# Performance work log

Hardware: AMD Instinct MI355X
Metric: run time of the kernel (lower is better)

The kernel has to match this reference:

```python
import jax, jax.numpy as jnp
import numpy as np

B, NSEQ, SEQ_PER = 2, 4, 256
S = NSEQ * SEQ_PER            # total sequence (stocks interleaved along seq dim)
D, H, HD = 1024, 16, 64       # d_model, nhead, head_dim
HD2, HD4 = HD // 2, HD // 4
DFF = 4096
LAMBDA_INIT = 0.2             # lambda_init_fn(0) = 0.8 - 0.6*exp(0)
SCALING = 1.0 / float(np.sqrt(HD2))
EPS_DEF = float(np.finfo(np.float32).eps)   # torch RMSNorm default eps (eps=None)
EPS_ATTN = 1e-5


def _rms(x, w, eps):
    return x * jax.lax.rsqrt(jnp.mean(x * x, axis=-1, keepdims=True) + eps) * w


def _rope(x, fc):
    # x: (B, T, NSEQ, 2H, HD2); fc: (T, HD4, 2) holding (cos, sin)
    xr = x.reshape(x.shape[:-1] + (HD4, 2))
    c = fc[None, :, None, None, :, 0]
    s = fc[None, :, None, None, :, 1]
    x0, x1 = xr[..., 0], xr[..., 1]
    return jnp.stack([x0 * c - x1 * s, x0 * s + x1 * c], axis=-1).reshape(x.shape)


def setup_inputs():
    key = jax.random.key(0)
    ks = jax.random.split(key, 16)
    def w(i, shape, std=0.02):
        return jax.random.normal(ks[i], shape, jnp.float32) * std
    # true RoPE table for seq_per_stock-1 positions
    t = jnp.arange(SEQ_PER - 1, dtype=jnp.float32)[:, None]
    inv = 1.0 / (10000.0 ** (jnp.arange(HD4, dtype=jnp.float32) / HD4))
    ang = t * inv[None, :]
    return {
        "x": jax.random.normal(ks[0], (B, S, D), jnp.float32),
        "freqs_cis": jnp.stack([jnp.cos(ang), jnp.sin(ang)], axis=-1),
        "w_norm1": jnp.ones((D,), jnp.float32),
        "w_norm2": jnp.ones((D,), jnp.float32),
        "Wq": w(1, (H * HD, D)), "bq": jnp.zeros((H * HD,), jnp.float32),
        "Wk": w(2, (H * HD, D)), "bk": jnp.zeros((H * HD,), jnp.float32),
        "Wv": w(3, (H * HD, D)), "bv": jnp.zeros((H * HD,), jnp.float32),
        "Wo": w(4, (D, H * HD)), "bo": jnp.zeros((D,), jnp.float32),
        "lq1": w(5, (HD2,), 0.1), "lk1": w(6, (HD2,), 0.1),
        "lq2": w(7, (HD2,), 0.1), "lk2": w(8, (HD2,), 0.1),
        "w_attn_norm": jnp.ones((HD,), jnp.float32),
        "Wg": w(9, (2 * DFF, D)), "bg": jnp.zeros((2 * DFF,), jnp.float32),
        "Wout": w(10, (D, DFF)), "bout": jnp.zeros((D,), jnp.float32),
    }


def reference(x, freqs_cis, w_norm1, w_norm2, Wq, bq, Wk, bk, Wv, bv, Wo, bo,
              lq1, lk1, lq2, lk2, w_attn_norm, Wg, bg, Wout, bout):
    Bz, Sz, _ = x.shape
    h = _rms(x, w_norm1, EPS_DEF)
    q = (h @ Wq.T + bq).reshape(Bz, SEQ_PER, NSEQ, 2 * H, HD2)
    k = (h @ Wk.T + bk).reshape(Bz, SEQ_PER, NSEQ, 2 * H, HD2)
    v = (h @ Wv.T + bv).reshape(Bz, Sz, H, HD).transpose(0, 2, 1, 3)   # (B,H,S,HD), interleaved order
    # RoPE on all but the first per-stock timestep; same freqs for every stock
    q = jnp.concatenate([q[:, :1], _rope(q[:, 1:], freqs_cis)], axis=1)
    k = jnp.concatenate([k[:, :1], _rope(k[:, 1:], freqs_cis)], axis=1)
    # reorder q/k to stock-major flat sequence (torch permute(0,4,1,2,3)+reshape)
    q = q.transpose(0, 2, 1, 3, 4).reshape(Bz, Sz, 2 * H, HD2).transpose(0, 2, 1, 3)
    k = k.transpose(0, 2, 1, 3, 4).reshape(Bz, Sz, 2 * H, HD2).transpose(0, 2, 1, 3)
    scores = jnp.einsum('bhqd,bhkd->bhqk', q, k) * SCALING              # (B,2H,S,S)
    causal = jnp.triu(jnp.ones((SEQ_PER, SEQ_PER), bool), 1)
    mask = jnp.tile(causal, (NSEQ, NSEQ))   # block-tiled causal, as torch .repeat
    att = jnp.sign(scores) * jax.nn.softmax(
        jnp.where(mask, -1e30, jnp.abs(scores)), axis=-1)
    lam = jnp.exp(jnp.sum(lk1 * lq1)) - jnp.exp(jnp.sum(lk2 * lq2)) + LAMBDA_INIT
    att = att.reshape(Bz, H, 2, Sz, Sz)
    a1, a2 = att[:, :, 0], att[:, :, 1]
    G = jnp.mean(a1, axis=-2, keepdims=True)          # mean over queries, broadcast back
    a = jnp.where(mask, 0.0, a1 - lam * a2 + lam * G)
    ao = jnp.einsum('bhqk,bhkd->bhqd', a, v)          # v kept in interleaved order (faithful to source)
    ao = _rms(ao, w_attn_norm, EPS_ATTN)
    ao = ao.reshape(Bz, Sz, H * HD)  # flat reinterpret (B,H,S,HD)->(B,S,H*HD), matches torch reshape chain
    x = x + ao @ Wo.T + bo
    h2 = _rms(x, w_norm2, EPS_DEF)
    u, vg = jnp.split(h2 @ Wg.T + bg, 2, axis=-1)
    return x + (u * jax.nn.silu(vg)) @ Wout.T + bout
```

## Files before the change

### kernel.cpp

```cpp
#include <hip/hip_runtime.h>

#define LAMBDA_INIT 0.2f
#define SCALING 0.17677669529663687f
#define EPS_DEF 1.1920928955078125e-07f
#define EPS_ATTN 1e-5f

typedef unsigned short us4 __attribute__((ext_vector_type(4)));
typedef unsigned short us8v __attribute__((ext_vector_type(8)));
typedef float f32x4 __attribute__((ext_vector_type(4)));
typedef float f32x2 __attribute__((ext_vector_type(2)));
typedef __bf16 bf16x8 __attribute__((ext_vector_type(8)));

#define MFMA16(a, b, c) __builtin_amdgcn_mfma_f32_16x16x32_bf16((a), (b), (c), 0, 0, 0)

__device__ __forceinline__ float bf2f(unsigned short u) {
    unsigned int x = ((unsigned int)u) << 16;
    return __builtin_bit_cast(float, x);
}
__device__ __forceinline__ unsigned short f2bf(float f) {
    unsigned int x = __builtin_bit_cast(unsigned int, f);
    x += 0x7fffu + ((x >> 16) & 1u);
    return (unsigned short)(x >> 16);
}
__device__ __forceinline__ void split8(f32x4 a, f32x4 b, us8v& hi, us8v& lo) {
#pragma unroll
    for (int u = 0; u < 4; u++) {
        unsigned short h = f2bf(a[u]);
        hi[u] = h; lo[u] = f2bf(a[u] - bf2f(h));
        unsigned short h2 = f2bf(b[u]);
        hi[4 + u] = h2; lo[4 + u] = f2bf(b[u] - bf2f(h2));
    }
}
__device__ __forceinline__ bf16x8 ldb(const unsigned short* p) {
    return __builtin_bit_cast(bf16x8, *(const us8v*)p);
}

__device__ __forceinline__ float wave_sum(float v) {
#pragma unroll
    for (int o = 32; o > 0; o >>= 1) v += __shfl_down(v, o);
    return v;
}
__device__ __forceinline__ float block_sum(float v, float* red4) {
    int wv = threadIdx.x >> 6;
    float w = wave_sum(v);
    __syncthreads();
    if ((threadIdx.x & 63) == 0) red4[wv] = w;
    __syncthreads();
    return red4[0] + red4[1] + red4[2] + red4[3];
}

__global__ __launch_bounds__(256) void prep(float* __restrict__ G, float* __restrict__ lamp,
                                            const float* lq1, const float* lk1,
                                            const float* lq2, const float* lk2) {
    int i = (blockIdx.x * 256 + threadIdx.x) * 4;
    G[i] = 0.f; G[i + 1] = 0.f; G[i + 2] = 0.f; G[i + 3] = 0.f;
    if (blockIdx.x == 0 && threadIdx.x == 0) {
        float a = 0.f, c = 0.f;
        for (int d = 0; d < 32; d++) {
            a += lq1[d] * lk1[d];
            c += lq2[d] * lk2[d];
        }
        *lamp = expf(a) - expf(c) + LAMBDA_INIT;
    }
}

__global__ __launch_bounds__(256) void cvt_bf16(const float* __restrict__ s,
                                                unsigned short* __restrict__ d, int n4) {
    int i = blockIdx.x * 256 + threadIdx.x;
    if (i >= n4) return;
    f32x4 v = ((const f32x4*)s)[i];
    us4 o;
#pragma unroll
    for (int u = 0; u < 4; u++) o[u] = f2bf(v[u]);
    ((us4*)d)[i] = o;
}

__global__ __launch_bounds__(256) void cvt_split3(
        const float* __restrict__ s0, const float* __restrict__ s1, const float* __restrict__ s2,
        unsigned short* __restrict__ h0, unsigned short* __restrict__ l0,
        unsigned short* __restrict__ h1p, unsigned short* __restrict__ l1p,
        unsigned short* __restrict__ h2p, unsigned short* __restrict__ l2p, int n4) {
    const int z = blockIdx.y;
    const float* s = (z == 0) ? s0 : (z == 1) ? s1 : s2;
    unsigned short* hi = (z == 0) ? h0 : (z == 1) ? h1p : h2p;
    unsigned short* lo = (z == 0) ? l0 : (z == 1) ? l1p : l2p;
    int i = blockIdx.x * 256 + threadIdx.x;
    if (i >= n4) return;
    f32x4 v = ((const f32x4*)s)[i];
    us4 h, l;
#pragma unroll
    for (int u = 0; u < 4; u++) {
        h[u] = f2bf(v[u]);
        l[u] = f2bf(v[u] - bf2f(h[u]));
    }
    ((us4*)hi)[i] = h;
    ((us4*)lo)[i] = l;
}

template <int OUTBF>
__global__ __launch_bounds__(256) void rms_kernel(const float* __restrict__ x,
                                                  const float* __restrict__ w,
                                                  void* __restrict__ out, float eps) {
    int row = blockIdx.x;
    int tid = threadIdx.x;
    size_t base = (size_t)row * 1024 + tid * 4;
    f32x4 v = *(const f32x4*)(x + base);
    float ss = v[0]*v[0] + v[1]*v[1] + v[2]*v[2] + v[3]*v[3];
    __shared__ float red4[4];
    float tot = block_sum(ss, red4);
    float r = rsqrtf(tot * (1.0f / 1024.f) + eps);
    f32x4 wv = *(const f32x4*)(w + tid * 4);
    if (OUTBF) {
        us4 o;
#pragma unroll
        for (int i = 0; i < 4; i++) o[i] = f2bf(v[i] * r * wv[i]);
        *(us4*)((unsigned short*)out + base) = o;
    } else {
        f32x4 o;
#pragma unroll
        for (int i = 0; i < 4; i++) o[i] = v[i] * r * wv[i];
        *(f32x4*)((float*)out + base) = o;
    }
}

__global__ __launch_bounds__(256) void rms_split(const float* __restrict__ x,
                                                 const float* __restrict__ w,
                                                 unsigned short* __restrict__ hh,
                                                 unsigned short* __restrict__ hl, float eps) {
    int row = blockIdx.x;
    int tid = threadIdx.x;
    size_t base = (size_t)row * 1024 + tid * 4;
    f32x4 v = *(const f32x4*)(x + base);
    float ss = v[0]*v[0] + v[1]*v[1] + v[2]*v[2] + v[3]*v[3];
    __shared__ float red4[4];
    float tot = block_sum(ss, red4);
    float r = rsqrtf(tot * (1.0f / 1024.f) + eps);
    f32x4 wv = *(const f32x4*)(w + tid * 4);
    us4 oh, ol;
#pragma unroll
    for (int i = 0; i < 4; i++) {
        float val = v[i] * r * wv[i];
        oh[i] = f2bf(val);
        ol[i] = f2bf(val - bf2f(oh[i]));
    }
    *(us4*)(hh + base) = oh;
    *(us4*)(hl + base) = ol;
}

__global__ __launch_bounds__(256) void gemm_qkv_ps(
        const unsigned short* __restrict__ AH, const unsigned short* __restrict__ AL,
        const unsigned short* __restrict__ WqH, const unsigned short* __restrict__ WqL,
        const unsigned short* __restrict__ WkH, const unsigned short* __restrict__ WkL,
        const unsigned short* __restrict__ WvH, const unsigned short* __restrict__ WvL,
        const float* __restrict__ bq, const float* __restrict__ bk, const float* __restrict__ bv,
        float* __restrict__ Yq, float* __restrict__ Yk, float* __restrict__ Yv) {
    const int z = blockIdx.z;
    const unsigned short* BH = (z == 0) ? WqH : (z == 1) ? WkH : WvH;
    const unsigned short* BL = (z == 0) ? WqL : (z == 1) ? WkL : WvL;
    const float* bias = (z == 0) ? bq : (z == 1) ? bk : bv;
    float* out        = (z == 0) ? Yq : (z == 1) ? Yk : Yv;
    const int K = 1024, N = 1024;
    __shared__ __align__(16) unsigned short Ah[64][72];
    __shared__ __align__(16) unsigned short Al[64][72];
    __shared__ __align__(16) unsigned short Bh[64][72];
    __shared__ __align__(16) unsigned short Bl[64][72];
    const int t = threadIdx.x;
    const int bm = blockIdx.x, bn = blockIdx.y;
    const int lane = t & 63, w = t >> 6;
    const int wr = w >> 1, wc = w & 1;
    const int l15 = lane & 15, lg = lane >> 4;
    const int sr = t >> 2, sc = (t & 3) * 16;

    const unsigned short* AgH = AH + (size_t)(bm * 64 + sr) * K + sc;
    const unsigned short* AgL = AL + (size_t)(bm * 64 + sr) * K + sc;
    const unsigned short* BgH = BH + (size_t)(bn * 64 + sr) * K + sc;
    const unsigned short* BgL = BL + (size_t)(bn * 64 + sr) * K + sc;

    f32x4 acc[2][2] = {};

    us8v ah0 = *(const us8v*)AgH, ah1 = *(const us8v*)(AgH + 8);
    us8v al0 = *(const us8v*)AgL, al1 = *(const us8v*)(AgL + 8);
    us8v bh0 = *(const us8v*)BgH, bh1 = *(const us8v*)(BgH + 8);
    us8v bl0 = *(const us8v*)BgL, bl1 = *(const us8v*)(BgL + 8);

    for (int k0 = 0; k0 < K; k0 += 64) {
        __syncthreads();
        *(us8v*)&Ah[sr][sc] = ah0; *(us8v*)&Ah[sr][sc + 8] = ah1;
        *(us8v*)&Al[sr][sc] = al0; *(us8v*)&Al[sr][sc + 8] = al1;
        *(us8v*)&Bh[sr][sc] = bh0; *(us8v*)&Bh[sr][sc + 8] = bh1;
        *(us8v*)&Bl[sr][sc] = bl0; *(us8v*)&Bl[sr][sc + 8] = bl1;
        __syncthreads();
        if (k0 + 64 < K) {
            const int kn = k0 + 64;
            ah0 = *(const us8v*)(AgH + kn); ah1 = *(const us8v*)(AgH + kn + 8);
            al0 = *(const us8v*)(AgL + kn); al1 = *(const us8v*)(AgL + kn + 8);
            bh0 = *(const us8v*)(BgH + kn); bh1 = *(const us8v*)(BgH + kn + 8);
            bl0 = *(const us8v*)(BgL + kn); bl1 = *(const us8v*)(BgL + kn + 8);
        }
#pragma unroll
        for (int kk = 0; kk < 2; kk++) {
            bf16x8 afh[2], afl[2], bfh[2], bfl[2];
#pragma unroll
            for (int mi = 0; mi < 2; mi++) {
                afh[mi] = ldb(&Ah[wr * 32 + mi * 16 + l15][kk * 32 + lg * 8]);
                afl[mi] = ldb(&Al[wr * 32 + mi * 16 + l15][kk * 32 + lg * 8]);
            }
#pragma unroll
            for (int ni = 0; ni < 2; ni++) {
                bfh[ni] = ldb(&Bh[wc * 32 + ni * 16 + l15][kk * 32 + lg * 8]);
                bfl[ni] = ldb(&Bl[wc * 32 + ni * 16 + l15][kk * 32 + lg * 8]);
            }
#pragma unroll
            for (int mi = 0; mi < 2; mi++)
#pragma unroll
                for (int ni = 0; ni < 2; ni++) {
                    acc[mi][ni] = MFMA16(afl[mi], bfh[ni], acc[mi][ni]);
                    acc[mi][ni] = MFMA16(afh[mi], bfl[ni], acc[mi][ni]);
                    acc[mi][ni] = MFMA16(afh[mi], bfh[ni], acc[mi][ni]);
                }
        }
    }

    const int rbase = bm * 64 + wr * 32 + (lg << 2);
    const int cbase = bn * 64 + wc * 32 + l15;
#pragma unroll
    for (int mi = 0; mi < 2; mi++) {
#pragma unroll
        for (int ni = 0; ni < 2; ni++) {
            int col = cbase + ni * 16;
            float bb = bias[col];
#pragma unroll
            for (int r = 0; r < 4; r++) {
                int row = rbase + mi * 16 + r;
                out[(size_t)row * N + col] = acc[mi][ni][r] + bb;
            }
        }
    }
}

__global__ __launch_bounds__(256) void gemm_mfma_wb(const unsigned short* __restrict__ A,
                                                    const unsigned short* __restrict__ Bt,
                                                    const float* __restrict__ bias,
                                                    const float* __restrict__ res,
                                                    float* __restrict__ out,
                                                    int M, int N, int K) {
    __shared__ __align__(16) unsigned short As[64][72];
    __shared__ __align__(16) unsigned short Bs[64][72];
    const int t = threadIdx.x;
    const int bm = blockIdx.x, bn = blockIdx.y;
    const int lane = t & 63, w = t >> 6;
    const int wr = w >> 1, wc = w & 1;
    const int l15 = lane & 15, lg = lane >> 4;
    const int sr = t >> 2, sc = (t & 3) * 16;

    const unsigned short* Ag = A + (size_t)(bm * 64 + sr) * K + sc;
    const unsigned short* Bg = Bt + (size_t)(bn * 64 + sr) * K + sc;

    f32x4 acc[2][2] = {};

    us8v a0 = *(const us8v*)Ag, a1 = *(const us8v*)(Ag + 8);
    us8v b0 = *(const us8v*)Bg, b1 = *(const us8v*)(Bg + 8);

    for (int k0 = 0; k0 < K; k0 += 64) {
        __syncthreads();
        *(us8v*)&As[sr][sc]     = a0;
        *(us8v*)&As[sr][sc + 8] = a1;
        *(us8v*)&Bs[sr][sc]     = b0;
        *(us8v*)&Bs[sr][sc + 8] = b1;
        __syncthreads();
        if (k0 + 64 < K) {
            const int kn = k0 + 64;
            a0 = *(const us8v*)(Ag + kn); a1 = *(const us8v*)(Ag + kn + 8);
            b0 = *(const us8v*)(Bg + kn); b1 = *(const us8v*)(Bg + kn + 8);
        }
#pragma unroll
        for (int kk = 0; kk < 2; kk++) {
            bf16x8 af[2], bf[2];
#pragma unroll
            for (int mi = 0; mi < 2; mi++)
                af[mi] = ldb(&As[wr * 32 + mi * 16 + l15][kk * 32 + lg * 8]);
#pragma unroll
            for (int ni = 0; ni < 2; ni++)
                bf[ni] = ldb(&Bs[wc * 32 + ni * 16 + l15][kk * 32 + lg * 8]);
#pragma unroll
            for (int mi = 0; mi < 2; mi++)
#pragma unroll
                for (int ni = 0; ni < 2; ni++)
                    acc[mi][ni] = MFMA16(af[mi], bf[ni], acc[mi][ni]);
        }
    }

    const int rbase = bm * 64 + wr * 32 + (lg << 2);
    const int cbase = bn * 64 + wc * 32 + l15;
#pragma unroll
    for (int mi = 0; mi < 2; mi++) {
#pragma unroll
        for (int ni = 0; ni < 2; ni++) {
            int col = cbase + ni * 16;
            float bb = bias[col];
#pragma unroll
            for (int r = 0; r < 4; r++) {
                int row = rbase + mi * 16 + r;
                size_t oi = (size_t)row * N + col;
                out[oi] = acc[mi][ni][r] + bb + res[oi];
            }
        }
    }
}

__global__ __launch_bounds__(256) void gemm_gate_wb(const unsigned short* __restrict__ A,
                                                    const unsigned short* __restrict__ WuB,
                                                    const unsigned short* __restrict__ WvB,
                                                    const float* __restrict__ bg,
                                                    unsigned short* __restrict__ mlp) {
    __shared__ __align__(16) unsigned short As[128][72];
    __shared__ __align__(16) unsigned short BsU[64][72];
    __shared__ __align__(16) unsigned short BsV[64][72];
    const int t = threadIdx.x;
    const int bm = blockIdx.x, bn = blockIdx.y;
    const int lane = t & 63, w = t >> 6;
    const int wr = w >> 1, wc = w & 1;
    const int l15 = lane & 15, lg = lane >> 4;
    const int sr = t >> 2, sc = (t & 3) * 16;

    const unsigned short* Ag  = A + (size_t)(bm * 128 + sr) * 1024 + sc;
    const unsigned short* Ag2 = Ag + (size_t)64 * 1024;
    const unsigned short* BgU = WuB + (size_t)(bn * 64 + sr) * 1024 + sc;
    const unsigned short* BgV = WvB + (size_t)(bn * 64 + sr) * 1024 + sc;

    f32x4 accU[4][2] = {};
    f32x4 accV[4][2] = {};

    us8v a0 = *(const us8v*)Ag,  a1 = *(const us8v*)(Ag + 8);
    us8v a2 = *(const us8v*)Ag2, a3 = *(const us8v*)(Ag2 + 8);
    us8v u0 = *(const us8v*)BgU, u1 = *(const us8v*)(BgU + 8);
    us8v v0 = *(const us8v*)BgV, v1 = *(const us8v*)(BgV + 8);

    for (int k0 = 0; k0 < 1024; k0 += 64) {
        __syncthreads();
        *(us8v*)&As[sr][sc]          = a0;
        *(us8v*)&As[sr][sc + 8]      = a1;
        *(us8v*)&As[sr + 64][sc]     = a2;
        *(us8v*)&As[sr + 64][sc + 8] = a3;
        *(us8v*)&BsU[sr][sc]         = u0;
        *(us8v*)&BsU[sr][sc + 8]     = u1;
        *(us8v*)&BsV[sr][sc]         = v0;
        *(us8v*)&BsV[sr][sc + 8]     = v1;
        __syncthreads();
        if (k0 + 64 < 1024) {
            const int kn = k0 + 64;
            a0 = *(const us8v*)(Ag + kn);  a1 = *(const us8v*)(Ag + kn + 8);
            a2 = *(const us8v*)(Ag2 + kn); a3 = *(const us8v*)(Ag2 + kn + 8);
            u0 = *(const us8v*)(BgU + kn); u1 = *(const us8v*)(BgU + kn + 8);
            v0 = *(const us8v*)(BgV + kn); v1 = *(const us8v*)(BgV + kn + 8);
        }
#pragma unroll
        for (int kk = 0; kk < 2; kk++) {
            bf16x8 af[4], bu[2], bv2[2];
#pragma unroll
            for (int mi = 0; mi < 4; mi++)
                af[mi] = ldb(&As[wr * 64 + mi * 16 + l15][kk * 32 + lg * 8]);
#pragma unroll
            for (int ni = 0; ni < 2; ni++) {
                bu[ni]  = ldb(&BsU[wc * 32 + ni * 16 + l15][kk * 32 + lg * 8]);
                bv2[ni] = ldb(&BsV[wc * 32 + ni * 16 + l15][kk * 32 + lg * 8]);
            }
#pragma unroll
            for (int mi = 0; mi < 4; mi++)
#pragma unroll
                for (int ni = 0; ni < 2; ni++) {
                    accU[mi][ni] = MFMA16(af[mi], bu[ni], accU[mi][ni]);
                    accV[mi][ni] = MFMA16(af[mi], bv2[ni], accV[mi][ni]);
                }
        }
    }

    const int rbase = bm * 128 + wr * 64 + (lg << 2);
    const int cbase = bn * 64 + wc * 32 + l15;
#pragma unroll
    for (int mi = 0; mi < 4; mi++) {
#pragma unroll
        for (int ni = 0; ni < 2; ni++) {
            int col = cbase + ni * 16;
            float bu_ = bg[col], bv_ = bg[4096 + col];
#pragma unroll
            for (int r = 0; r < 4; r++) {
                int row = rbase + mi * 16 + r;
                float u = accU[mi][ni][r] + bu_;
                float v = accV[mi][ni][r] + bv_;
                float s = v / (1.f + __expf(-v));
                mlp[(size_t)row * 4096 + col] = f2bf(u * s);
            }
        }
    }
}

__global__ __launch_bounds__(256) void rope_inplace(float* __restrict__ Y,
                                                    const float* __restrict__ fc) {
    int t = blockIdx.x;
    int s = t & 1023;
    int p = s >> 2;
    if (p == 0) return;
    int c0 = threadIdx.x * 4;
    float* y = Y + (size_t)t * 1024 + c0;
    int d4 = (c0 & 31) >> 1;
    f32x4 f = *(const f32x4*)(fc + ((size_t)(p - 1) * 16 + d4) * 2);
    float v0 = y[0], v1 = y[1], v2 = y[2], v3 = y[3];
    y[0] = v0 * f[0] - v1 * f[1];
    y[1] = v0 * f[1] + v1 * f[0];
    y[2] = v2 * f[2] - v3 * f[3];
    y[3] = v2 * f[3] + v3 * f[2];
}

__global__ __launch_bounds__(256) void rope_split_k(const float* __restrict__ Yk,
                                                    const float* __restrict__ fc,
                                                    unsigned short* __restrict__ KhG,
                                                    unsigned short* __restrict__ KlG) {
    int t = blockIdx.x;
    int s = t & 1023;
    int p = s >> 2;
    int c0 = threadIdx.x * 4;
    const float* y = Yk + (size_t)t * 1024 + c0;
    float v0 = y[0], v1 = y[1], v2 = y[2], v3 = y[3];
    if (p > 0) {
        int d4 = (c0 & 31) >> 1;
        f32x4 f = *(const f32x4*)(fc + ((size_t)(p - 1) * 16 + d4) * 2);
        float w0 = v0 * f[0] - v1 * f[1];
        float w1 = v0 * f[1] + v1 * f[0];
        float w2 = v2 * f[2] - v3 * f[3];
        float w3 = v2 * f[3] + v3 * f[2];
        v0 = w0; v1 = w1; v2 = w2; v3 = w3;
    }
    us4 hi, lo;
    hi[0] = f2bf(v0); lo[0] = f2bf(v0 - bf2f(hi[0]));
    hi[1] = f2bf(v1); lo[1] = f2bf(v1 - bf2f(hi[1]));
    hi[2] = f2bf(v2); lo[2] = f2bf(v2 - bf2f(hi[2]));
    hi[3] = f2bf(v3); lo[3] = f2bf(v3 - bf2f(hi[3]));
    *(us4*)(KhG + (size_t)t * 1024 + c0) = hi;
    *(us4*)(KlG + (size_t)t * 1024 + c0) = lo;
}

__global__ __launch_bounds__(256) void v_split_t(const float* __restrict__ Yv,
                                                 unsigned short* __restrict__ VtH,
                                                 unsigned short* __restrict__ VtL) {
    const int jc = blockIdx.x, h = blockIdx.y, b = blockIdx.z;
    __shared__ float tile[64][65];
    const int t = threadIdx.x;
    {
        const int jr = t >> 2, dc = (t & 3) * 16;
        const float* src = Yv + ((size_t)(b * 1024 + jc * 64 + jr) << 10) + h * 64 + dc;
        *(f32x4*)&tile[jr][dc]      = *(const f32x4*)src;
        *(f32x4*)&tile[jr][dc + 4]  = *(const f32x4*)(src + 4);
        *(f32x4*)&tile[jr][dc + 8]  = *(const f32x4*)(src + 8);
        *(f32x4*)&tile[jr][dc + 12] = *(const f32x4*)(src + 12);
    }
    __syncthreads();
    const int d = t >> 2, js = (t & 3) * 16;
    us8v h0, h1, l0, l1;
#pragma unroll
    for (int n = 0; n < 16; n++) {
        float val = tile[js + n][d];
        unsigned short hh = f2bf(val);
        unsigned short ll = f2bf(val - bf2f(hh));
        if (n < 8) { h0[n] = hh; l0[n] = ll; }
        else       { h1[n - 8] = hh; l1[n - 8] = ll; }
    }
    size_t ob = (((size_t)(b * 16 + h) * 64 + d) << 10) + jc * 64 + js;
    *(us8v*)(VtH + ob) = h0; *(us8v*)(VtH + ob + 8) = h1;
    *(us8v*)(VtL + ob) = l0; *(us8v*)(VtL + ob + 8) = l1;
}

__global__ __launch_bounds__(256) void pass_1(const float* __restrict__ Yq,
                                              const unsigned short* __restrict__ KhG,
                                              const unsigned short* __restrict__ KlG,
                                              const unsigned short* __restrict__ VtH,
                                              const unsigned short* __restrict__ VtL,
                                              const float* __restrict__ lamp,
                                              float* __restrict__ G,
                                              float* __restrict__ AOp) {
    const int blk = blockIdx.x;
    const int qc = 15 - (blk >> 5);
    const int h  = blk & 15;
    const int b  = (blk >> 4) & 1;
    const int t = threadIdx.x;
    const int lane = t & 63, w = t >> 6;
    const int l15 = lane & 15, lg = lane >> 4;

    __shared__ __align__(16) unsigned short Kh[64][72];
    __shared__ __align__(16) unsigned short Kl[64][72];
    __shared__ __align__(16) unsigned short Vth[64][72];
    __shared__ __align__(16) unsigned short Vtl[64][72];
    __shared__ __align__(16) unsigned short Wh[64][72];
    __shared__ __align__(16) unsigned short Wl[64][72];
    __shared__ float Gacc[4][1024];

    for (int i = t; i < 4096; i += 256) ((float*)Gacc)[i] = 0.f;

    us8v qh[2], ql[2];
    {
        const float* qp = Yq + ((size_t)(b * 1024 + qc * 64 + w * 16 + l15) << 10)
                          + h * 64 + lg * 8;
#pragma unroll
        for (int H = 0; H < 2; H++)
            split8(*(const f32x4*)(qp + H * 32), *(const f32x4*)(qp + H * 32 + 4), qh[H], ql[H]);
    }
    const int dq0 = w * 16 + (lg << 2);

    const int srow = t >> 2, ssub = t & 3;
    const int ptk = 4 * (srow & 15) + (srow >> 4);
    const unsigned short* KhB = KhG + ((size_t)(b * 1024) << 10) + h * 64;
    const unsigned short* KlB = KlG + ((size_t)(b * 1024) << 10) + h * 64;
    const unsigned short* VhB = VtH + (((size_t)(b * 16 + h) * 64 + srow) << 10) + ssub * 256;
    const unsigned short* VlB = VtL + (((size_t)(b * 16 + h) * 64 + srow) << 10) + ssub * 256;
    const float lam = *lamp;

    float z1r[4] = {0.f, 0.f, 0.f, 0.f};
    float z2r[4] = {0.f, 0.f, 0.f, 0.f};

    us8v rkh0, rkh1, rkl0, rkl1;
    {
        const unsigned short* kh = KhB + ((size_t)ptk << 10) + ssub * 16;
        const unsigned short* kl = KlB + ((size_t)ptk << 10) + ssub * 16;
        rkh0 = *(const us8v*)kh; rkh1 = *(const us8v*)(kh + 8);
        rkl0 = *(const us8v*)kl; rkl1 = *(const us8v*)(kl + 8);
    }
    for (int kc = 0; kc <= qc; kc++) {
        __syncthreads();
        *(us8v*)&Kh[srow][ssub * 16]     = rkh0;
        *(us8v*)&Kh[srow][ssub * 16 + 8] = rkh1;
        *(us8v*)&Kl[srow][ssub * 16]     = rkl0;
        *(us8v*)&Kl[srow][ssub * 16 + 8] = rkl1;
        __syncthreads();
        if (kc < qc) {
            const unsigned short* kh = KhB + ((size_t)((kc + 1) * 64 + ptk) << 10) + ssub * 16;
            const unsigned short* kl = KlB + ((size_t)((kc + 1) * 64 + ptk) << 10) + ssub * 16;
            rkh0 = *(const us8v*)kh; rkh1 = *(const us8v*)(kh + 8);
            rkl0 = *(const us8v*)kl; rkl1 = *(const us8v*)(kl + 8);
        }
        const int kpos = kc * 16 + l15;
#pragma unroll
        for (int kf = 0; kf < 4; kf++) {
            const int krow = kf * 16 + l15;
            const int kcol = lg * 8;
            bf16x8 b1h = ldb(&Kh[krow][kcol]),      b1l = ldb(&Kl[krow][kcol]);
            bf16x8 b2h = ldb(&Kh[krow][32 + kcol]), b2l = ldb(&Kl[krow][32 + kcol]);
            f32x4 s1 = {}, s2 = {};
            s1 = MFMA16(__builtin_bit_cast(bf16x8, ql[0]), b1h, s1);
            s1 = MFMA16(__builtin_bit_cast(bf16x8, qh[0]), b1l, s1);
            s1 = MFMA16(__builtin_bit_cast(bf16x8, qh[0]), b1h, s1);
            s2 = MFMA16(__builtin_bit_cast(bf16x8, ql[1]), b2h, s2);
            s2 = MFMA16(__builtin_bit_cast(bf16x8, qh[1]), b2l, s2);
            s2 = MFMA16(__builtin_bit_cast(bf16x8, qh[1]), b2h, s2);
#pragma unroll
            for (int r = 0; r < 4; r++) {
                int pq = (qc * 64 + dq0 + r) >> 2;
                if (kpos <= pq) {
                    z1r[r] += __expf(fabsf(s1[r] * SCALING));
                    z2r[r] += __expf(fabsf(s2[r] * SCALING));
                }
            }
        }
    }
#pragma unroll
    for (int r = 0; r < 4; r++) {
        float a = z1r[r];
        a += __shfl_xor(a, 1); a += __shfl_xor(a, 2);
        a += __shfl_xor(a, 4); a += __shfl_xor(a, 8);
        z1r[r] = 1.f / fmaxf(a, 1e-20f);
        float c = z2r[r];
        c += __shfl_xor(c, 1); c += __shfl_xor(c, 2);
        c += __shfl_xor(c, 4); c += __shfl_xor(c, 8);
        z2r[r] = 1.f / fmaxf(c, 1e-20f);
    }

    f32x4 ao[4] = {};

    us8v rvh0, rvh1, rvl0, rvl1;
    {
        const unsigned short* kh = KhB + ((size_t)ptk << 10) + ssub * 16;
        const unsigned short* kl = KlB + ((size_t)ptk << 10) + ssub * 16;
        rkh0 = *(const us8v*)kh; rkh1 = *(const us8v*)(kh + 8);
        rkl0 = *(const us8v*)kl; rkl1 = *(const us8v*)(kl + 8);
        rvh0 = *(const us8v*)VhB; rvh1 = *(const us8v*)(VhB + 8);
        rvl0 = *(const us8v*)VlB; rvl1 = *(const us8v*)(VlB + 8);
    }
    for (int kc = 0; kc <= qc; kc++) {
        __syncthreads();
        *(us8v*)&Kh[srow][ssub * 16]      = rkh0;
        *(us8v*)&Kh[srow][ssub * 16 + 8]  = rkh1;
        *(us8v*)&Kl[srow][ssub * 16]      = rkl0;
        *(us8v*)&Kl[srow][ssub * 16 + 8]  = rkl1;
        *(us8v*)&Vth[srow][ssub * 16]     = rvh0;
        *(us8v*)&Vth[srow][ssub * 16 + 8] = rvh1;
        *(us8v*)&Vtl[srow][ssub * 16]     = rvl0;
        *(us8v*)&Vtl[srow][ssub * 16 + 8] = rvl1;
        __syncthreads();
        if (kc < qc) {
            const unsigned short* kh = KhB + ((size_t)((kc + 1) * 64 + ptk) << 10) + ssub * 16;
            const unsigned short* kl = KlB + ((size_t)((kc + 1) * 64 + ptk) << 10) + ssub * 16;
            rkh0 = *(const us8v*)kh; rkh1 = *(const us8v*)(kh + 8);
            rkl0 = *(const us8v*)kl; rkl1 = *(const us8v*)(kl + 8);
            const unsigned short* vh = VhB + (kc + 1) * 16;
            const unsigned short* vl = VlB + (kc + 1) * 16;
            rvh0 = *(const us8v*)vh; rvh1 = *(const us8v*)(vh + 8);
            rvl0 = *(const us8v*)vl; rvl1 = *(const us8v*)(vl + 8);
        }
        const int kpos = kc * 16 + l15;
#pragma unroll
        for (int kf = 0; kf < 4; kf++) {
            const int krow = kf * 16 + l15;
            const int kcol = lg * 8;
            bf16x8 b1h = ldb(&Kh[krow][kcol]),      b1l = ldb(&Kl[krow][kcol]);
            bf16x8 b2h = ldb(&Kh[krow][32 + kcol]), b2l = ldb(&Kl[krow][32 + kcol]);
            f32x4 s1 = {}, s2 = {};
            s1 = MFMA16(__builtin_bit_cast(bf16x8, ql[0]), b1h, s1);
            s1 = MFMA16(__builtin_bit_cast(bf16x8, qh[0]), b1l, s1);
            s1 = MFMA16(__builtin_bit_cast(bf16x8, qh[0]), b1h, s1);
            s2 = MFMA16(__builtin_bit_cast(bf16x8, ql[1]), b2h, s2);
            s2 = MFMA16(__builtin_bit_cast(bf16x8, qh[1]), b2l, s2);
            s2 = MFMA16(__builtin_bit_cast(bf16x8, qh[1]), b2h, s2);
            const int kli = kf * 16 + l15;
            float colsum = 0.f;
#pragma unroll
            for (int r = 0; r < 4; r++) {
                int pq = (qc * 64 + dq0 + r) >> 2;
                float wv = 0.f, a1 = 0.f;
                if (kpos <= pq) {
                    float t1 = s1[r] * SCALING, t2 = s2[r] * SCALING;
                    float sg1 = (t1 > 0.f) ? 1.f : ((t1 < 0.f) ? -1.f : 0.f);
                    float sg2 = (t2 > 0.f) ? 1.f : ((t2 < 0.f) ? -1.f : 0.f);
                    a1 = sg1 * __expf(fabsf(t1)) * z1r[r];
                    wv = a1 - lam * (sg2 * __expf(fabsf(t2)) * z2r[r]);
                }
                colsum += a1;
                unsigned short hh = f2bf(wv);
                Wh[dq0 + r][kli] = hh;
                Wl[dq0 + r][kli] = f2bf(wv - bf2f(hh));
            }
            colsum += __shfl_xor(colsum, 16);
            colsum += __shfl_xor(colsum, 32);
            if (lane < 16) Gacc[w][kf * 256 + kc * 16 + lane] = colsum;
        }
#pragma unroll
        for (int kh2 = 0; kh2 < 2; kh2++) {
            bf16x8 wah = ldb(&Wh[w * 16 + l15][kh2 * 32 + lg * 8]);
            bf16x8 wal = ldb(&Wl[w * 16 + l15][kh2 * 32 + lg * 8]);
#pragma unroll
            for (int df = 0; df < 4; df++) {
                bf16x8 vbh = ldb(&Vth[df * 16 + l15][kh2 * 32 + lg * 8]);
                bf16x8 vbl = ldb(&Vtl[df * 16 + l15][kh2 * 32 + lg * 8]);
                ao[df] = MFMA16(wah, vbl, ao[df]);
                ao[df] = MFMA16(wal, vbh, ao[df]);
                ao[df] = MFMA16(wah, vbh, ao[df]);
            }
        }
    }

#pragma unroll
    for (int df = 0; df < 4; df++) {
#pragma unroll
        for (int r = 0; r < 4; r++) {
            int tq = qc * 64 + dq0 + r;
            int qrow = ((tq & 3) << 8) + (tq >> 2);
            AOp[((((size_t)(b * 16 + h)) << 10) + qrow) * 64 + df * 16 + l15] = ao[df][r];
        }
    }

    __syncthreads();
    float* Gb = G + ((size_t)(b * 16 + h) << 10);
    const int limp = (qc + 1) << 4;
    for (int idx = t; idx < 1024; idx += 256) {
        if ((idx & 255) < limp) {
            float s = Gacc[0][idx] + Gacc[1][idx] + Gacc[2][idx] + Gacc[3][idx];
            atomicAdd(&Gb[idx], s);
        }
    }
}

__global__ __launch_bounds__(256) void pass_2a(const float* __restrict__ G,
                                               const float* __restrict__ Yv,
                                               float* __restrict__ GVpre) {
    const int h = blockIdx.x, b = blockIdx.y;
    const int t = threadIdx.x;
    __shared__ float Gl[1024];
    __shared__ float S[256][64];
    __shared__ float segsum[4][64];
    for (int i = t; i < 1024; i += 256) Gl[i] = G[((size_t)(b * 16 + h) << 10) + i];
    __syncthreads();
    const int d = t & 63, pg = t >> 6;
    const float* Yvb = Yv + ((size_t)b << 20) + h * 64 + d;
    for (int p0 = 0; p0 < 64; p0++) {
        int pos = pg * 64 + p0;
        float s = 0.f;
#pragma unroll
        for (int sq = 0; sq < 4; sq++) {
            int j = (sq << 8) + pos;
            s += Gl[j] * Yvb[(size_t)j << 10];
        }
        S[pos][d] = s;
    }
    __syncthreads();
    float acc = 0.f;
    for (int p0 = 0; p0 < 64; p0++) {
        int pos = pg * 64 + p0;
        acc += S[pos][d];
        S[pos][d] = acc;
    }
    segsum[pg][d] = acc;
    __syncthreads();
    float off = 0.f;
    for (int g = 0; g < pg; g++) off += segsum[g][d];
    float* gv = GVpre + (((size_t)(b * 16 + h)) << 14) + d;
    for (int p0 = 0; p0 < 64; p0++) {
        int pos = pg * 64 + p0;
        gv[pos << 6] = S[pos][d] + off;
    }
}

__global__ __launch_bounds__(256) void pass_2b(const float* __restrict__ AOp,
                                               const float* __restrict__ GVpre,
                                               const float* __restrict__ lamp,
                                               const float* __restrict__ wan,
                                               unsigned short* __restrict__ aoS) {
    const int qg = blockIdx.x;
    const int h = blockIdx.y, b = blockIdx.z;
    const int t = threadIdx.x;
    const int d = t & 63, rg = t >> 6;
    const float lamg = (*lamp) * (1.f / 1024.f);
    const float wv = wan[d];
    const float* aob = AOp + ((((size_t)(b * 16 + h)) << 10) + (qg << 8)) * 64 + d;
    const float* gvb = GVpre + (((size_t)(b * 16 + h)) << 14) + d;
    unsigned short* ob = aoS + ((size_t)b << 20) + ((size_t)h << 16) + ((size_t)(qg << 8) << 6) + d;
    for (int p0 = 0; p0 < 64; p0++) {
        int pq = p0 * 4 + rg;
        float ao = aob[(size_t)pq << 6] + lamg * gvb[(size_t)pq << 6];
        float ss = ao * ao;
#pragma unroll
        for (int o = 1; o < 64; o <<= 1) ss += __shfl_xor(ss, o);
        float rr_ = rsqrtf(ss * (1.f / 64.f) + EPS_ATTN);
        ob[(size_t)pq << 6] = f2bf(ao * rr_ * wv);
    }
}

extern "C" void kernel_launch(void* const* d_in, const int* in_sizes, int n_in,
                              void* d_out, int out_size, void* d_ws, size_t ws_size,
                              hipStream_t stream) {
    const float* x    = (const float*)d_in[0];
    const float* fc   = (const float*)d_in[1];
    const float* w1   = (const float*)d_in[2];
    const float* w2   = (const float*)d_in[3];
    const float* Wq   = (const float*)d_in[4];
    const float* bq   = (const float*)d_in[5];
    const float* Wk   = (const float*)d_in[6];
    const float* bk   = (const float*)d_in[7];
    const float* Wv   = (const float*)d_in[8];
    const float* bv   = (const float*)d_in[9];
    const float* Wo   = (const float*)d_in[10];
    const float* bo   = (const float*)d_in[11];
    const float* lq1  = (const float*)d_in[12];
    const float* lk1  = (const float*)d_in[13];
    const float* lq2  = (const float*)d_in[14];
    const float* lk2  = (const float*)d_in[15];
    const float* wan  = (const float*)d_in[16];
    const float* Wg   = (const float*)d_in[17];
    const float* bg   = (const float*)d_in[18];
    const float* Wout = (const float*)d_in[19];
    const float* bout = (const float*)d_in[20];

    char* ws = (char*)d_ws;
    const size_t MB = 1024 * 1024;
    float* G    = (float*)(ws);
    float* lam  = (float*)(ws + 256 * 1024);
    unsigned short* hH = (unsigned short*)(ws + 1 * MB);
    unsigned short* hL = (unsigned short*)(ws + 5 * MB);
    float* Yq   = (float*)(ws + 9 * MB);
    float* Yk   = (float*)(ws + 17 * MB);
    float* Yv   = (float*)(ws + 25 * MB);
    unsigned short* WqH = (unsigned short*)(ws + 33 * MB);
    unsigned short* WqL = (unsigned short*)(ws + 35 * MB);
    unsigned short* WkH = (unsigned short*)(ws + 37 * MB);
    unsigned short* WkL = (unsigned short*)(ws + 39 * MB);
    unsigned short* WvH = (unsigned short*)(ws + 41 * MB);
    unsigned short* WvL = (unsigned short*)(ws + 43 * MB);
    float* AOp  = (float*)(ws + 33 * MB);
    float* GVpre= (float*)(ws + 41 * MB);
    unsigned short* WoB = (unsigned short*)(ws + 43 * MB);
    unsigned short* KhG = (unsigned short*)(ws + 1 * MB);
    unsigned short* KlG = (unsigned short*)(ws + 5 * MB);
    unsigned short* VtH = (unsigned short*)(ws + 17 * MB);
    unsigned short* VtL = (unsigned short*)(ws + 21 * MB);
    unsigned short* aoS = (unsigned short*)(ws + 1 * MB);
    float* X1           = (float*)(ws + 9 * MB);
    unsigned short* h2b = (unsigned short*)(ws + 5 * MB);
    unsigned short* mlp = (unsigned short*)(ws + 17 * MB);
    unsigned short* WuB = (unsigned short*)(ws + 33 * MB);
    unsigned short* WvB2= (unsigned short*)(ws + 41 * MB);
    unsigned short* WoutB=(unsigned short*)(ws + 33 * MB);

    prep<<<32, 256, 0, stream>>>(G, lam, lq1, lk1, lq2, lk2);
    rms_split<<<2048, 256, 0, stream>>>(x, w1, hH, hL, EPS_DEF);
    cvt_split3<<<dim3(1024, 3), 256, 0, stream>>>(Wq, Wk, Wv, WqH, WqL, WkH, WkL, WvH, WvL, 262144);
    gemm_qkv_ps<<<dim3(32, 16, 3), 256, 0, stream>>>(hH, hL, WqH, WqL, WkH, WkL, WvH, WvL,
                                                     bq, bk, bv, Yq, Yk, Yv);
    cvt_bf16<<<1024, 256, 0, stream>>>(Wo, WoB, 262144);
    rope_inplace<<<2048, 256, 0, stream>>>(Yq, fc);
    rope_split_k<<<2048, 256, 0, stream>>>(Yk, fc, KhG, KlG);
    v_split_t<<<dim3(16, 16, 2), 256, 0, stream>>>(Yv, VtH, VtL);
    pass_1<<<512, 256, 0, stream>>>(Yq, KhG, KlG, VtH, VtL, lam, G, AOp);
    pass_2a<<<dim3(16, 2), 256, 0, stream>>>(G, Yv, GVpre);
    pass_2b<<<dim3(4, 16, 2), 256, 0, stream>>>(AOp, GVpre, lam, wan, aoS);
    dim3 gmf(32, 16);
    gemm_mfma_wb<<<gmf, 256, 0, stream>>>(aoS, WoB, bo, x, X1, 2048, 1024, 1024);
    cvt_bf16<<<4096, 256, 0, stream>>>(Wg, WuB, 1048576);
    cvt_bf16<<<4096, 256, 0, stream>>>(Wg + 4194304, WvB2, 1048576);
    rms_kernel<1><<<2048, 256, 0, stream>>>(X1, w2, h2b, EPS_DEF);
    gemm_gate_wb<<<dim3(16, 64), 256, 0, stream>>>(h2b, WuB, WvB2, bg, mlp);
    cvt_bf16<<<4096, 256, 0, stream>>>(Wout, WoutB, 1048576);
    gemm_mfma_wb<<<gmf, 256, 0, stream>>>(mlp, WoutB, bout, X1, (float*)d_out, 2048, 1024, 4096);
}
```

Measured before the change: 422.2 us.

## Split attention into normalizer pass and output pass, fuse Q RoPE into both

The old pass_1 kernel did two things: a first loop that summed the softmax normalizers, then a loop that built the attention output. The first loop now lives in a separate pass_0 kernel that writes the row sums to a small MZ buffer; pass_1 reads them back. pass_0 needs far less shared memory, so more of its blocks can run at once. The standalone rope_inplace kernel is removed and RoPE is applied to Q when it is loaded in both passes, at the cost of an extra kernel launch and recomputing the Q split and rotation twice.

```diff
diff --git a/kernel.cpp b/kernel.cpp
--- a/kernel.cpp
+++ b/kernel.cpp
@@ -33,6 +33,17 @@
 }
 __device__ __forceinline__ bf16x8 ldb(const unsigned short* p) {
     return __builtin_bit_cast(bf16x8, *(const us8v*)p);
+}
+__device__ __forceinline__ f32x4 rope4(f32x4 v, const float* __restrict__ fc, int p, int dd) {
+    if (p == 0) return v;
+    int d4 = (dd & 31) >> 1;
+    f32x4 f = *(const f32x4*)(fc + ((size_t)(p - 1) * 16 + d4) * 2);
+    f32x4 o;
+    o[0] = v[0] * f[0] - v[1] * f[1];
+    o[1] = v[0] * f[1] + v[1] * f[0];
+    o[2] = v[2] * f[2] - v[3] * f[3];
+    o[3] = v[2] * f[3] + v[3] * f[2];
+    return o;
 }
 
 __device__ __forceinline__ float wave_sum(float v) {
@@ -395,23 +406,6 @@
     }
 }
 
-__global__ __launch_bounds__(256) void rope_inplace(float* __restrict__ Y,
-                                                    const float* __restrict__ fc) {
-    int t = blockIdx.x;
-    int s = t & 1023;
-    int p = s >> 2;
-    if (p == 0) return;
-    int c0 = threadIdx.x * 4;
-    float* y = Y + (size_t)t * 1024 + c0;
-    int d4 = (c0 & 31) >> 1;
-    f32x4 f = *(const f32x4*)(fc + ((size_t)(p - 1) * 16 + d4) * 2);
-    float v0 = y[0], v1 = y[1], v2 = y[2], v3 = y[3];
-    y[0] = v0 * f[0] - v1 * f[1];
-    y[1] = v0 * f[1] + v1 * f[0];
-    y[2] = v2 * f[2] - v3 * f[3];
-    y[3] = v2 * f[3] + v3 * f[2];
-}
-
 __global__ __launch_bounds__(256) void rope_split_k(const float* __restrict__ Yk,
                                                     const float* __restrict__ fc,
                                                     unsigned short* __restrict__ KhG,
@@ -470,14 +464,11 @@
     *(us8v*)(VtL + ob) = l0; *(us8v*)(VtL + ob + 8) = l1;
 }
 
-__global__ __launch_bounds__(256) void pass_1(const float* __restrict__ Yq,
+__global__ __launch_bounds__(256) void pass_0(const float* __restrict__ Yq,
+                                              const float* __restrict__ fc,
                                               const unsigned short* __restrict__ KhG,
                                               const unsigned short* __restrict__ KlG,
-                                              const unsigned short* __restrict__ VtH,
-                                              const unsigned short* __restrict__ VtL,
-                                              const float* __restrict__ lamp,
-                                              float* __restrict__ G,
-                                              float* __restrict__ AOp) {
+                                              float* __restrict__ MZ) {
     const int blk = blockIdx.x;
     const int qc = 15 - (blk >> 5);
     const int h  = blk & 15;
@@ -488,21 +479,19 @@
 
     __shared__ __align__(16) unsigned short Kh[64][72];
     __shared__ __align__(16) unsigned short Kl[64][72];
-    __shared__ __align__(16) unsigned short Vth[64][72];
-    __shared__ __align__(16) unsigned short Vtl[64][72];
-    __shared__ __align__(16) unsigned short Wh[64][72];
-    __shared__ __align__(16) unsigned short Wl[64][72];
-    __shared__ float Gacc[4][1024];
-
-    for (int i = t; i < 4096; i += 256) ((float*)Gacc)[i] = 0.f;
 
     us8v qh[2], ql[2];
     {
-        const float* qp = Yq + ((size_t)(b * 1024 + qc * 64 + w * 16 + l15) << 10)
-                          + h * 64 + lg * 8;
-#pragma unroll
-        for (int H = 0; H < 2; H++)
-            split8(*(const f32x4*)(qp + H * 32), *(const f32x4*)(qp + H * 32 + 4), qh[H], ql[H]);
+        const int srq = qc * 64 + w * 16 + l15;
+        const int p = srq >> 2;
+        const float* qp = Yq + ((size_t)(b * 1024 + srq) << 10) + h * 64 + lg * 8;
+#pragma unroll
+        for (int H = 0; H < 2; H++) {
+            int dd = lg * 8 + H * 32;
+            f32x4 a = rope4(*(const f32x4*)(qp + H * 32), fc, p, dd);
+            f32x4 c = rope4(*(const f32x4*)(qp + H * 32 + 4), fc, p, dd + 4);
+            split8(a, c, qh[H], ql[H]);
+        }
     }
     const int dq0 = w * 16 + (lg << 2);
 
@@ -510,9 +499,6 @@
     const int ptk = 4 * (srow & 15) + (srow >> 4);
     const unsigned short* KhB = KhG + ((size_t)(b * 1024) << 10) + h * 64;
     const unsigned short* KlB = KlG + ((size_t)(b * 1024) << 10) + h * 64;
-    const unsigned short* VhB = VtH + (((size_t)(b * 16 + h) * 64 + srow) << 10) + ssub * 256;
-    const unsigned short* VlB = VtL + (((size_t)(b * 16 + h) * 64 + srow) << 10) + ssub * 256;
-    const float lam = *lamp;
 
     float z1r[4] = {0.f, 0.f, 0.f, 0.f};
     float z2r[4] = {0.f, 0.f, 0.f, 0.f};
@@ -566,16 +552,80 @@
         float a = z1r[r];
         a += __shfl_xor(a, 1); a += __shfl_xor(a, 2);
         a += __shfl_xor(a, 4); a += __shfl_xor(a, 8);
-        z1r[r] = 1.f / fmaxf(a, 1e-20f);
         float c = z2r[r];
         c += __shfl_xor(c, 1); c += __shfl_xor(c, 2);
         c += __shfl_xor(c, 4); c += __shfl_xor(c, 8);
-        z2r[r] = 1.f / fmaxf(c, 1e-20f);
-    }
+        if (l15 == 0) {
+            int s2i = qc * 64 + dq0 + r;
+            f32x2 zz; zz[0] = a; zz[1] = c;
+            *(f32x2*)(MZ + (((size_t)(b * 16 + h) << 10) + s2i) * 2) = zz;
+        }
+    }
+}
+
+__global__ __launch_bounds__(256) void pass_1(const float* __restrict__ Yq,
+                                              const float* __restrict__ fc,
+                                              const unsigned short* __restrict__ KhG,
+                                              const unsigned short* __restrict__ KlG,
+                                              const unsigned short* __restrict__ VtH,
+                                              const unsigned short* __restrict__ VtL,
+                                              const float* __restrict__ MZ,
+                                              const float* __restrict__ lamp,
+                                              float* __restrict__ G,
+                                              float* __restrict__ AOp) {
+    const int blk = blockIdx.x;
+    const int qc = 15 - (blk >> 5);
+    const int h  = blk & 15;
+    const int b  = (blk >> 4) & 1;
+    const int t = threadIdx.x;
+    const int lane = t & 63, w = t >> 6;
+    const int l15 = lane & 15, lg = lane >> 4;
+
+    __shared__ __align__(16) unsigned short Kh[64][72];
+    __shared__ __align__(16) unsigned short Kl[64][72];
+    __shared__ __align__(16) unsigned short Vth[64][72];
+    __shared__ __align__(16) unsigned short Vtl[64][72];
+    __shared__ __align__(16) unsigned short Wh[64][72];
+    __shared__ __align__(16) unsigned short Wl[64][72];
+    __shared__ float Gacc[4][1024];
+
+    for (int i = t; i < 4096; i += 256) ((float*)Gacc)[i] = 0.f;
+
+    us8v qh[2], ql[2];
+    {
+        const int srq = qc * 64 + w * 16 + l15;
+        const int p = srq >> 2;
+        const float* qp = Yq + ((size_t)(b * 1024 + srq) << 10) + h * 64 + lg * 8;
+#pragma unroll
+        for (int H = 0; H < 2; H++) {
+            int dd = lg * 8 + H * 32;
+            f32x4 a = rope4(*(const f32x4*)(qp + H * 32), fc, p, dd);
+            f32x4 c = rope4(*(const f32x4*)(qp + H * 32 + 4), fc, p, dd + 4);
+            split8(a, c, qh[H], ql[H]);
+        }
+    }
+    const int dq0 = w * 16 + (lg << 2);
+
+    float z1r[4], z2r[4];
+#pragma unroll
+    for (int r = 0; r < 4; r++) {
+        int s2i = qc * 64 + dq0 + r;
+        f32x2 zz = *(const f32x2*)(MZ + (((size_t)(b * 16 + h) << 10) + s2i) * 2);
+        z1r[r] = 1.f / fmaxf(zz[0], 1e-20f);
+        z2r[r] = 1.f / fmaxf(zz[1], 1e-20f);
+    }
+
+    const int srow = t >> 2, ssub = t & 3;
+    const int ptk = 4 * (srow & 15) + (srow >> 4);
+    const unsigned short* KhB = KhG + ((size_t)(b * 1024) << 10) + h * 64;
+    const unsigned short* KlB = KlG + ((size_t)(b * 1024) << 10) + h * 64;
+    const unsigned short* VhB = VtH + (((size_t)(b * 16 + h) * 64 + srow) << 10) + ssub * 256;
+    const unsigned short* VlB = VtL + (((size_t)(b * 16 + h) * 64 + srow) << 10) + ssub * 256;
+    const float lam = *lamp;
 
     f32x4 ao[4] = {};
 
-    us8v rvh0, rvh1, rvl0, rvl1;
+    us8v rkh0, rkh1, rkl0, rkl1, rvh0, rvh1, rvl0, rvl1;
     {
         const unsigned short* kh = KhB + ((size_t)ptk << 10) + ssub * 16;
         const unsigned short* kl = KlB + ((size_t)ptk << 10) + ssub * 16;
@@ -771,6 +821,7 @@
     const size_t MB = 1024 * 1024;
     float* G    = (float*)(ws);
     float* lam  = (float*)(ws + 256 * 1024);
+    float* MZ   = (float*)(ws + 384 * 1024);
     unsigned short* hH = (unsigned short*)(ws + 1 * MB);
     unsigned short* hL = (unsigned short*)(ws + 5 * MB);
     float* Yq   = (float*)(ws + 9 * MB);
@@ -803,10 +854,10 @@
     gemm_qkv_ps<<<dim3(32, 16, 3), 256, 0, stream>>>(hH, hL, WqH, WqL, WkH, WkL, WvH, WvL,
                                                      bq, bk, bv, Yq, Yk, Yv);
     cvt_bf16<<<1024, 256, 0, stream>>>(Wo, WoB, 262144);
-    rope_inplace<<<2048, 256, 0, stream>>>(Yq, fc);
     rope_split_k<<<2048, 256, 0, stream>>>(Yk, fc, KhG, KlG);
     v_split_t<<<dim3(16, 16, 2), 256, 0, stream>>>(Yv, VtH, VtL);
-    pass_1<<<512, 256, 0, stream>>>(Yq, KhG, KlG, VtH, VtL, lam, G, AOp);
+    pass_0<<<512, 256, 0, stream>>>(Yq, fc, KhG, KlG, MZ);
+    pass_1<<<512, 256, 0, stream>>>(Yq, fc, KhG, KlG, VtH, VtL, MZ, lam, G, AOp);
     pass_2a<<<dim3(16, 2), 256, 0, stream>>>(G, Yv, GVpre);
     pass_2b<<<dim3(4, 16, 2), 256, 0, stream>>>(AOp, GVpre, lam, wan, aoS);
     dim3 gmf(32, 16);
```

Measured after the change: 422.0 us. Within noise of the previous version (-0.0%).
